# Performance work log

Measured on AMD Instinct MI355X. Metric: run time of the kernel, lower is better.

The kernel has to match this reference:

```python
import jax, jax.numpy as jnp
import numpy as np

B, S, D_MODEL, N_HEADS = 2, 256, 512, 8
HEAD_DIM = D_MODEL // N_HEADS  # 64; k.size(-1) used for scaling


def setup_inputs() -> dict:
    key = jax.random.key(0)
    ks = jax.random.split(key, 11)
    sd = 1.0 / np.sqrt(D_MODEL)
    sf = 1.0 / np.sqrt(N_HEADS * D_MODEL)
    return {
        "Q": jax.random.normal(ks[0], (B, S, D_MODEL), jnp.float32),
        "K": jax.random.normal(ks[1], (B, S, D_MODEL), jnp.float32),
        "V": jax.random.normal(ks[2], (B, S, D_MODEL), jnp.float32),
        "Wq": jax.random.normal(ks[3], (D_MODEL, D_MODEL * N_HEADS), jnp.float32) * sd,
        "bq": jax.random.normal(ks[4], (D_MODEL * N_HEADS,), jnp.float32) * sd,
        "Wk": jax.random.normal(ks[5], (D_MODEL, D_MODEL * N_HEADS), jnp.float32) * sd,
        "bk": jax.random.normal(ks[6], (D_MODEL * N_HEADS,), jnp.float32) * sd,
        "Wv": jax.random.normal(ks[7], (D_MODEL, D_MODEL * N_HEADS), jnp.float32) * sd,
        "bv": jax.random.normal(ks[8], (D_MODEL * N_HEADS,), jnp.float32) * sd,
        "Wf": jax.random.normal(ks[9], (N_HEADS * D_MODEL, D_MODEL), jnp.float32) * sf,
        "bf": jax.random.normal(ks[10], (D_MODEL,), jnp.float32) * sf,
    }


def _split_heads(x):
    # Faithful to torch: view(B, -1, n_heads, d_model//n_heads).transpose(1, 2).
    # x: (B, S, D_MODEL*N_HEADS) -> (B, N_HEADS, S*N_HEADS, HEAD_DIM)
    b = x.shape[0]
    return jnp.transpose(x.reshape(b, -1, N_HEADS, HEAD_DIM), (0, 2, 1, 3))


def reference(Q, K, V, Wq, bq, Wk, bk, Wv, bv, Wf, bf):
    q = _split_heads(Q @ Wq + bq)  # (B, H, S*H, Dh)
    k = _split_heads(K @ Wk + bk)
    v = _split_heads(V @ Wv + bv)
    scale = 1.0 / jnp.sqrt(jnp.float32(HEAD_DIM))
    scores = jnp.einsum("bhqd,bhkd->bhqk", q, k) * scale  # (B, H, S*H, S*H)
    weights = jax.nn.softmax(scores, axis=-1)
    ctx = jnp.einsum("bhqk,bhkd->bhqd", weights, v)  # (B, H, S*H, Dh)
    # transpose(1,2).view(B, -1, n_heads*d_model) -> (B, S, N_HEADS*D_MODEL)
    ctx = jnp.transpose(ctx, (0, 2, 1, 3)).reshape(Q.shape[0], -1, N_HEADS * D_MODEL)
    return ctx @ Wf + bf  # (B, S, D_MODEL)
```

## Files before the change

### kernel.cpp

```cpp
#include <hip/hip_runtime.h>
#include <hip/hip_bf16.h>


typedef __attribute__((ext_vector_type(4))) float f32x4;
typedef __attribute__((ext_vector_type(8))) short short8;
typedef __attribute__((ext_vector_type(4))) short short4v;
typedef __attribute__((ext_vector_type(4))) unsigned int u32x4;

#define SEQ 2048
#define DH 64
#define BH 16
#define ROWS 512
#define DM 512
#define NQ 4096
#define KSPLIT 8

static __device__ __forceinline__ unsigned short f2bf(float f) {
    return __builtin_bit_cast(unsigned short, __float2bfloat16(f));
}
static __device__ __forceinline__ short4v pk4(float a, float b, float c, float d) {
    return short4v{(short)f2bf(a), (short)f2bf(b), (short)f2bf(c), (short)f2bf(d)};
}
static __device__ __forceinline__ unsigned cvt_pk_bf16(float lo, float hi) {
    unsigned r;
    asm("v_cvt_pk_bf16_f32 %0, %1, %2" : "=v"(r) : "v"(lo), "v"(hi));
    return r;
}

__global__ __launch_bounds__(256) void qkv_proj_kernel(
    const float* __restrict__ Q, const float* __restrict__ K, const float* __restrict__ V,
    const float* __restrict__ Wq, const float* __restrict__ bq,
    const float* __restrict__ Wk, const float* __restrict__ bk,
    const float* __restrict__ Wv, const float* __restrict__ bv,
    unsigned short* __restrict__ q_bf, unsigned short* __restrict__ k_bf,
    unsigned short* __restrict__ vT_bf)
{
    const int mat = blockIdx.z;
    const float* X    = (mat == 0) ? Q  : (mat == 1) ? K  : V;
    const float* W    = (mat == 0) ? Wq : (mat == 1) ? Wk : Wv;
    const float* bias = (mat == 0) ? bq : (mat == 1) ? bk : bv;

    const int n0 = blockIdx.x * 64;
    const int m0 = blockIdx.y * 64;
    const int tid = threadIdx.x;
    const int w = tid >> 6, l = tid & 63;
    const int lr = l & 15, lg = l >> 4;

    __shared__ unsigned short a_lds[64][72];
    __shared__ unsigned short wt_lds[64 * 72];

    const int xr0 = tid >> 4, xc4 = (tid & 15) * 4;
    const int wn = tid & 63, wkseg = tid >> 6;
    const int wxr = (wn >> 3) & 7;

    f32x4 acc[4];
#pragma unroll
    for (int ct = 0; ct < 4; ++ct) acc[ct] = f32x4{0.f, 0.f, 0.f, 0.f};

    float4 rx[4];
    float rwv[16];

#pragma unroll
    for (int i = 0; i < 4; ++i)
        rx[i] = *reinterpret_cast<const float4*>(X + (m0 + i * 16 + xr0) * DM + xc4);
#pragma unroll
    for (int j = 0; j < 16; ++j)
        rwv[j] = W[(size_t)(wkseg * 16 + j) * NQ + n0 + wn];

    for (int t = 0; t < 8; ++t) {
#pragma unroll
        for (int i = 0; i < 4; ++i)
            *reinterpret_cast<short4v*>(&a_lds[i * 16 + xr0][xc4]) =
                pk4(rx[i].x, rx[i].y, rx[i].z, rx[i].w);
#pragma unroll
        for (int j4 = 0; j4 < 4; ++j4) {
            int kb = wkseg * 2 + (j4 >> 1);
            int off = wn * 72 + ((kb ^ wxr) << 3) + (j4 & 1) * 4;
            *reinterpret_cast<short4v*>(&wt_lds[off]) =
                pk4(rwv[j4 * 4 + 0], rwv[j4 * 4 + 1], rwv[j4 * 4 + 2], rwv[j4 * 4 + 3]);
        }
        __syncthreads();

        if (t < 7) {
            int k0 = (t + 1) * 64;
#pragma unroll
            for (int i = 0; i < 4; ++i)
                rx[i] = *reinterpret_cast<const float4*>(X + (m0 + i * 16 + xr0) * DM + k0 + xc4);
#pragma unroll
            for (int j = 0; j < 16; ++j)
                rwv[j] = W[(size_t)(k0 + wkseg * 16 + j) * NQ + n0 + wn];
        }

#pragma unroll
        for (int ks = 0; ks < 2; ++ks) {
            short8 a = *reinterpret_cast<const short8*>(&a_lds[w * 16 + lr][ks * 32 + lg * 8]);
#pragma unroll
            for (int ct = 0; ct < 4; ++ct) {
                int row = ct * 16 + lr;
                int kb = ks * 4 + lg;
                short8 b = *reinterpret_cast<const short8*>(
                    &wt_lds[row * 72 + ((kb ^ ((row >> 3) & 7)) << 3)]);
                acc[ct] = __builtin_amdgcn_mfma_f32_16x16x32_bf16(a, b, acc[ct], 0, 0, 0);
            }
        }
        __syncthreads();
    }

#pragma unroll
    for (int ct = 0; ct < 4; ++ct) {
        int c = n0 + ct * 16 + lr;
        float bv_ = bias[c];
        int h = (c >> 6) & 7, d = c & 63, c1 = c >> 9;
#pragma unroll
        for (int r = 0; r < 4; ++r) {
            int row = m0 + w * 16 + lg * 4 + r;
            int b = row >> 8, s = row & 255;
            int n = s * 8 + c1;
            unsigned short bfv = f2bf(acc[ct][r] + bv_);
            if (mat == 0)      q_bf[((b * 8 + h) * SEQ + n) * DH + d] = bfv;
            else if (mat == 1) k_bf[((b * 8 + h) * SEQ + n) * DH + d] = bfv;
            else               vT_bf[((b * 8 + h) * DH + d) * SEQ + n] = bfv;
        }
    }
}

__global__ __launch_bounds__(512, 4) void attn_kernel(
    const unsigned short* __restrict__ q_bf,
    const unsigned short* __restrict__ k_bf,
    const unsigned short* __restrict__ vT_bf,
    unsigned short* __restrict__ ctx_bf)
{
    const int bh = blockIdx.y;
    const int b = bh >> 3, h = bh & 7;
    const int n0 = blockIdx.x * 64;
    const int tid = threadIdx.x;
    const int w = tid >> 6, l = tid & 63;
    const int wq = w & 3, half = w >> 2;
    const int lr = l & 15, lg = l >> 4;
    const int gtid = tid & 255;

    const unsigned short* qb = q_bf + (size_t)bh * SEQ * DH;
    const unsigned short* kb = k_bf + (size_t)bh * SEQ * DH;
    const unsigned short* vb = vT_bf + (size_t)bh * DH * SEQ;

    __shared__ __align__(16) unsigned short kvl[4][64][72];
    __shared__ float l_red[4][16];

    const int qrow = n0 + wq * 16 + lr;
    short8 aq[2];
    aq[0] = *reinterpret_cast<const short8*>(qb + qrow * DH + lg * 8);
    aq[1] = *reinterpret_cast<const short8*>(qb + qrow * DH + 32 + lg * 8);

    f32x4 o[4];
#pragma unroll
    for (int i = 0; i < 4; ++i) o[i] = f32x4{0.f, 0.f, 0.f, 0.f};
    float l_part = 0.f;

    const int srow = gtid >> 3, sc8 = (gtid & 7) * 8;
    const int kbase0 = half * (SEQ / 2);

    short8 rk[2], rv[2];
#pragma unroll
    for (int i = 0; i < 2; ++i) {
        int row = srow + i * 32;
        rk[i] = *reinterpret_cast<const short8*>(kb + (kbase0 + row) * DH + sc8);
        rv[i] = *reinterpret_cast<const short8*>(vb + row * SEQ + kbase0 + sc8);
    }

    const bool lowc  = (lg < 2);
    const bool sendR = (lg == 0) || (lg == 3);
    const bool oddlg = (lg & 1);

    for (int kt = 0; kt < SEQ / 2 / 64; ++kt) {
#pragma unroll
        for (int i = 0; i < 2; ++i) {
            *reinterpret_cast<short8*>(&kvl[half][srow + i * 32][sc8]) = rk[i];
            *reinterpret_cast<short8*>(&kvl[2 + half][srow + i * 32][sc8]) = rv[i];
        }
        __syncthreads();

        if (kt < SEQ / 2 / 64 - 1) {
            int kb0 = kbase0 + (kt + 1) * 64;
#pragma unroll
            for (int i = 0; i < 2; ++i) {
                int row = srow + i * 32;
                rk[i] = *reinterpret_cast<const short8*>(kb + (kb0 + row) * DH + sc8);
                rv[i] = *reinterpret_cast<const short8*>(vb + row * SEQ + kb0 + sc8);
            }
        }

        f32x4 s[4];
#pragma unroll
        for (int ct = 0; ct < 4; ++ct) s[ct] = f32x4{0.f, 0.f, 0.f, 0.f};
#pragma unroll
        for (int ks = 0; ks < 2; ++ks) {
#pragma unroll
            for (int ct = 0; ct < 4; ++ct) {
                short8 kfrag = *reinterpret_cast<const short8*>(&kvl[half][ct * 16 + lr][ks * 32 + lg * 8]);
                s[ct] = __builtin_amdgcn_mfma_f32_16x16x32_bf16(kfrag, aq[ks], s[ct], 0, 0, 0);
            }
        }

        float rs_t = 0.f;
#pragma unroll
        for (int ct = 0; ct < 4; ++ct)
#pragma unroll
            for (int r = 0; r < 4; ++r) {
                float pv = exp2f(s[ct][r] * 0.18033688011112042f);
                s[ct][r] = pv;
                rs_t += pv;
            }
        l_part += rs_t;

        unsigned Wp[8];
#pragma unroll
        for (int c = 0; c < 4; ++c) {
            Wp[c * 2 + 0] = cvt_pk_bf16(s[c][0], s[c][1]);
            Wp[c * 2 + 1] = cvt_pk_bf16(s[c][2], s[c][3]);
        }

        unsigned keepA[4], r1r[4];
#pragma unroll
        for (int a = 0; a < 2; ++a)
#pragma unroll
            for (int hh = 0; hh < 2; ++hh) {
                int i = a * 2 + hh;
                unsigned snd = lowc ? Wp[(2 * a + 1) * 2 + hh] : Wp[(2 * a) * 2 + hh];
                keepA[i]     = lowc ? Wp[(2 * a) * 2 + hh]     : Wp[(2 * a + 1) * 2 + hh];
                r1r[i] = (unsigned)__shfl_xor((int)snd, 32);
            }
        unsigned r2k[4], r2r[4];
#pragma unroll
        for (int i = 0; i < 4; ++i) {
            unsigned snd = sendR ? r1r[i] : keepA[i];
            r2k[i]       = sendR ? keepA[i] : r1r[i];
            r2r[i] = (unsigned)__shfl_xor((int)snd, 16);
        }

        u32x4 pbu[2];
#pragma unroll
        for (int ks = 0; ks < 2; ++ks) {
            unsigned g0a = oddlg ? r2r[2 * ks + 0] : r2k[2 * ks + 0];
            unsigned g0b = oddlg ? r2r[2 * ks + 1] : r2k[2 * ks + 1];
            unsigned g1a = oddlg ? r2k[2 * ks + 0] : r2r[2 * ks + 0];
            unsigned g1b = oddlg ? r2k[2 * ks + 1] : r2r[2 * ks + 1];
            pbu[ks] = u32x4{g0a, g0b, g1a, g1b};
        }

#pragma unroll
        for (int ks = 0; ks < 2; ++ks) {
            short8 pfrag = __builtin_bit_cast(short8, pbu[ks]);
#pragma unroll
            for (int dt = 0; dt < 4; ++dt) {
                short8 vfrag = *reinterpret_cast<const short8*>(&kvl[2 + half][dt * 16 + lr][ks * 32 + lg * 8]);
                o[dt] = __builtin_amdgcn_mfma_f32_16x16x32_bf16(vfrag, pfrag, o[dt], 0, 0, 0);
            }
        }
        __syncthreads();
    }

    float rs = l_part;
    rs += __shfl_xor(rs, 16);
    rs += __shfl_xor(rs, 32);

    float* o_red = (float*)&kvl[0][0][0];
    const int orow = (wq * 16 + lr) * 72;
    if (half == 1) {
#pragma unroll
        for (int dt = 0; dt < 4; ++dt)
            *reinterpret_cast<f32x4*>(&o_red[orow + dt * 16 + lg * 4]) = o[dt];
        if (lg == 0) l_red[wq][lr] = rs;
    }
    __syncthreads();
    if (half == 0) {
        float inv = 1.f / (rs + l_red[wq][lr]);
        int n = n0 + wq * 16 + lr;
        int sp = n >> 3;
        int cbase = (n & 7) * 512 + h * 64;
        unsigned short* dst = ctx_bf + (size_t)(b * 256 + sp) * NQ + cbase;
#pragma unroll
        for (int dt = 0; dt < 4; ++dt) {
            f32x4 oo = *reinterpret_cast<f32x4*>(&o_red[orow + dt * 16 + lg * 4]);
            oo = (o[dt] + oo) * inv;
            *reinterpret_cast<short4v*>(dst + dt * 16 + lg * 4) = pk4(oo[0], oo[1], oo[2], oo[3]);
        }
    }
}

__global__ __launch_bounds__(256) void out_proj_splitk_kernel(
    const unsigned short* __restrict__ ctx_bf,
    const float* __restrict__ Wf,
    float* __restrict__ part)
{
    const int n0 = blockIdx.x * 64;
    const int m0 = blockIdx.y * 64;
    const int ksplit = blockIdx.z;
    const int kbase = ksplit * (NQ / KSPLIT);
    const int tid = threadIdx.x;
    const int w = tid >> 6, l = tid & 63;
    const int lr = l & 15, lg = l >> 4;

    __shared__ unsigned short a_lds[64][72];
    __shared__ unsigned short wt_lds[64 * 72];

    const int arow0 = tid >> 3, ac8 = (tid & 7) * 8;
    const int wn = tid & 63, wkseg = tid >> 6;
    const int wxr = (wn >> 3) & 7;

    f32x4 acc[4];
#pragma unroll
    for (int ct = 0; ct < 4; ++ct) acc[ct] = f32x4{0.f, 0.f, 0.f, 0.f};

    short8 ra[2];
    float rwv[16];

    {
#pragma unroll
        for (int i = 0; i < 2; ++i)
            ra[i] = *reinterpret_cast<const short8*>(
                ctx_bf + (size_t)(m0 + arow0 + i * 32) * NQ + kbase + ac8);
#pragma unroll
        for (int j = 0; j < 16; ++j)
            rwv[j] = Wf[(size_t)(kbase + wkseg * 16 + j) * DM + n0 + wn];
    }

    for (int t = 0; t < 8; ++t) {
#pragma unroll
        for (int i = 0; i < 2; ++i)
            *reinterpret_cast<short8*>(&a_lds[arow0 + i * 32][ac8]) = ra[i];
#pragma unroll
        for (int j4 = 0; j4 < 4; ++j4) {
            int kb = wkseg * 2 + (j4 >> 1);
            int off = wn * 72 + ((kb ^ wxr) << 3) + (j4 & 1) * 4;
            *reinterpret_cast<short4v*>(&wt_lds[off]) =
                pk4(rwv[j4 * 4 + 0], rwv[j4 * 4 + 1], rwv[j4 * 4 + 2], rwv[j4 * 4 + 3]);
        }
        __syncthreads();

        if (t < 7) {
            int k0 = kbase + (t + 1) * 64;
#pragma unroll
            for (int i = 0; i < 2; ++i)
                ra[i] = *reinterpret_cast<const short8*>(
                    ctx_bf + (size_t)(m0 + arow0 + i * 32) * NQ + k0 + ac8);
#pragma unroll
            for (int j = 0; j < 16; ++j)
                rwv[j] = Wf[(size_t)(k0 + wkseg * 16 + j) * DM + n0 + wn];
        }

#pragma unroll
        for (int ks = 0; ks < 2; ++ks) {
            short8 a = *reinterpret_cast<const short8*>(&a_lds[w * 16 + lr][ks * 32 + lg * 8]);
#pragma unroll
            for (int ct = 0; ct < 4; ++ct) {
                int row = ct * 16 + lr;
                int kb = ks * 4 + lg;
                short8 b = *reinterpret_cast<const short8*>(
                    &wt_lds[row * 72 + ((kb ^ ((row >> 3) & 7)) << 3)]);
                acc[ct] = __builtin_amdgcn_mfma_f32_16x16x32_bf16(a, b, acc[ct], 0, 0, 0);
            }
        }
        __syncthreads();
    }

    float* pbase = part + (size_t)ksplit * ROWS * DM;
#pragma unroll
    for (int ct = 0; ct < 4; ++ct) {
        int c = n0 + ct * 16 + lr;
#pragma unroll
        for (int r = 0; r < 4; ++r) {
            int row = m0 + w * 16 + lg * 4 + r;
            pbase[(size_t)row * DM + c] = acc[ct][r];
        }
    }
}

__global__ __launch_bounds__(256) void out_reduce_kernel(
    const float* __restrict__ part, const float* __restrict__ bf_,
    float* __restrict__ out)
{
    int i4 = blockIdx.x * 256 + threadIdx.x;
    int e = i4 * 4;
    float4 acc = *reinterpret_cast<const float4*>(bf_ + (e & (DM - 1)));
#pragma unroll
    for (int ks = 0; ks < KSPLIT; ++ks) {
        float4 p = *reinterpret_cast<const float4*>(part + (size_t)ks * ROWS * DM + e);
        acc.x += p.x; acc.y += p.y; acc.z += p.z; acc.w += p.w;
    }
    *reinterpret_cast<float4*>(out + e) = acc;
}

extern "C" void kernel_launch(void* const* d_in, const int* in_sizes, int n_in,
                              void* d_out, int out_size, void* d_ws, size_t ws_size,
                              hipStream_t stream) {
    const float* Q  = (const float*)d_in[0];
    const float* K  = (const float*)d_in[1];
    const float* V  = (const float*)d_in[2];
    const float* Wq = (const float*)d_in[3];
    const float* bq = (const float*)d_in[4];
    const float* Wk = (const float*)d_in[5];
    const float* bk = (const float*)d_in[6];
    const float* Wv = (const float*)d_in[7];
    const float* bv = (const float*)d_in[8];
    const float* Wf = (const float*)d_in[9];
    const float* bf = (const float*)d_in[10];
    float* out = (float*)d_out;

    unsigned short* q_bf  = (unsigned short*)d_ws;
    unsigned short* k_bf  = q_bf + (size_t)BH * SEQ * DH;
    unsigned short* vT_bf = k_bf + (size_t)BH * SEQ * DH;
    unsigned short* ctx_bf = vT_bf + (size_t)BH * SEQ * DH;
    float* part = (float*)d_ws;

    qkv_proj_kernel<<<dim3(NQ / 64, ROWS / 64, 3), 256, 0, stream>>>(
        Q, K, V, Wq, bq, Wk, bk, Wv, bv, q_bf, k_bf, vT_bf);
    attn_kernel<<<dim3(SEQ / 64, BH), 512, 0, stream>>>(q_bf, k_bf, vT_bf, ctx_bf);
    out_proj_splitk_kernel<<<dim3(DM / 64, ROWS / 64, KSPLIT), 256, 0, stream>>>(
        ctx_bf, Wf, part);
    out_reduce_kernel<<<dim3(ROWS * DM / 4 / 256), 256, 0, stream>>>(part, bf, out);
}
```

Measured before the change: 87.07 us.

## Split attention KV range across four wave groups per block instead of two

The attention block grows from 512 to 1024 threads. The key/value sequence is split into four quarters, each processed by its own group of four waves with its own shared-memory K/V tiles. Partial outputs and row sums from the three extra quarters are reduced through shared memory by the first group. This halves each block's sequential KV loop and adds in-block parallelism, at the cost of more LDS per block (lower block occupancy) and a larger final reduction.

Measured after the change: 157.9 us. 81.4% more time.

```diff
diff --git a/kernel.cpp b/kernel.cpp
--- a/kernel.cpp
+++ b/kernel.cpp
@@ -124,7 +124,7 @@
     }
 }
 
-__global__ __launch_bounds__(512, 4) void attn_kernel(
+__global__ __launch_bounds__(1024, 8) void attn_kernel(
     const unsigned short* __restrict__ q_bf,
     const unsigned short* __restrict__ k_bf,
     const unsigned short* __restrict__ vT_bf,
@@ -135,7 +135,7 @@
     const int n0 = blockIdx.x * 64;
     const int tid = threadIdx.x;
     const int w = tid >> 6, l = tid & 63;
-    const int wq = w & 3, half = w >> 2;
+    const int wq = w & 3, qtr = w >> 2;
     const int lr = l & 15, lg = l >> 4;
     const int gtid = tid & 255;
 
@@ -143,8 +143,8 @@
     const unsigned short* kb = k_bf + (size_t)bh * SEQ * DH;
     const unsigned short* vb = vT_bf + (size_t)bh * DH * SEQ;
 
-    __shared__ __align__(16) unsigned short kvl[4][64][72];
-    __shared__ float l_red[4][16];
+    __shared__ __align__(16) unsigned short kvl[8][64][72];
+    __shared__ float l_red[3][4][16];
 
     const int qrow = n0 + wq * 16 + lr;
     short8 aq[2];
@@ -157,7 +157,7 @@
     float l_part = 0.f;
 
     const int srow = gtid >> 3, sc8 = (gtid & 7) * 8;
-    const int kbase0 = half * (SEQ / 2);
+    const int kbase0 = qtr * (SEQ / 4);
 
     short8 rk[2], rv[2];
 #pragma unroll
@@ -171,15 +171,15 @@
     const bool sendR = (lg == 0) || (lg == 3);
     const bool oddlg = (lg & 1);
 
-    for (int kt = 0; kt < SEQ / 2 / 64; ++kt) {
+    for (int kt = 0; kt < SEQ / 4 / 64; ++kt) {
 #pragma unroll
         for (int i = 0; i < 2; ++i) {
-            *reinterpret_cast<short8*>(&kvl[half][srow + i * 32][sc8]) = rk[i];
-            *reinterpret_cast<short8*>(&kvl[2 + half][srow + i * 32][sc8]) = rv[i];
-        }
-        __syncthreads();
-
-        if (kt < SEQ / 2 / 64 - 1) {
+            *reinterpret_cast<short8*>(&kvl[qtr][srow + i * 32][sc8]) = rk[i];
+            *reinterpret_cast<short8*>(&kvl[4 + qtr][srow + i * 32][sc8]) = rv[i];
+        }
+        __syncthreads();
+
+        if (kt < SEQ / 4 / 64 - 1) {
             int kb0 = kbase0 + (kt + 1) * 64;
 #pragma unroll
             for (int i = 0; i < 2; ++i) {
@@ -196,7 +196,7 @@
         for (int ks = 0; ks < 2; ++ks) {
 #pragma unroll
             for (int ct = 0; ct < 4; ++ct) {
-                short8 kfrag = *reinterpret_cast<const short8*>(&kvl[half][ct * 16 + lr][ks * 32 + lg * 8]);
+                short8 kfrag = *reinterpret_cast<const short8*>(&kvl[qtr][ct * 16 + lr][ks * 32 + lg * 8]);
                 s[ct] = __builtin_amdgcn_mfma_f32_16x16x32_bf16(kfrag, aq[ks], s[ct], 0, 0, 0);
             }
         }
@@ -252,7 +252,7 @@
             short8 pfrag = __builtin_bit_cast(short8, pbu[ks]);
 #pragma unroll
             for (int dt = 0; dt < 4; ++dt) {
-                short8 vfrag = *reinterpret_cast<const short8*>(&kvl[2 + half][dt * 16 + lr][ks * 32 + lg * 8]);
+                short8 vfrag = *reinterpret_cast<const short8*>(&kvl[4 + qtr][dt * 16 + lr][ks * 32 + lg * 8]);
                 o[dt] = __builtin_amdgcn_mfma_f32_16x16x32_bf16(vfrag, pfrag, o[dt], 0, 0, 0);
             }
         }
@@ -264,24 +264,29 @@
     rs += __shfl_xor(rs, 32);
 
     float* o_red = (float*)&kvl[0][0][0];
-    const int orow = (wq * 16 + lr) * 72;
-    if (half == 1) {
+    if (qtr != 0) {
+        const int base = ((qtr - 1) * 4 + wq) * (16 * 72) + lr * 72;
 #pragma unroll
         for (int dt = 0; dt < 4; ++dt)
-            *reinterpret_cast<f32x4*>(&o_red[orow + dt * 16 + lg * 4]) = o[dt];
-        if (lg == 0) l_red[wq][lr] = rs;
+            *reinterpret_cast<f32x4*>(&o_red[base + dt * 16 + lg * 4]) = o[dt];
+        if (lg == 0) l_red[qtr - 1][wq][lr] = rs;
     }
     __syncthreads();
-    if (half == 0) {
-        float inv = 1.f / (rs + l_red[wq][lr]);
+    if (qtr == 0) {
+        float l_tot = rs + l_red[0][wq][lr] + l_red[1][wq][lr] + l_red[2][wq][lr];
+        float inv = 1.f / l_tot;
         int n = n0 + wq * 16 + lr;
         int sp = n >> 3;
         int cbase = (n & 7) * 512 + h * 64;
         unsigned short* dst = ctx_bf + (size_t)(b * 256 + sp) * NQ + cbase;
+        const int rbase = wq * (16 * 72) + lr * 72;
 #pragma unroll
         for (int dt = 0; dt < 4; ++dt) {
-            f32x4 oo = *reinterpret_cast<f32x4*>(&o_red[orow + dt * 16 + lg * 4]);
-            oo = (o[dt] + oo) * inv;
+            f32x4 oo = o[dt];
+#pragma unroll
+            for (int p = 0; p < 3; ++p)
+                oo += *reinterpret_cast<f32x4*>(&o_red[p * 4 * (16 * 72) + rbase + dt * 16 + lg * 4]);
+            oo *= inv;
             *reinterpret_cast<short4v*>(dst + dt * 16 + lg * 4) = pk4(oo[0], oo[1], oo[2], oo[3]);
         }
     }
@@ -414,7 +419,7 @@
 
     qkv_proj_kernel<<<dim3(NQ / 64, ROWS / 64, 3), 256, 0, stream>>>(
         Q, K, V, Wq, bq, Wk, bk, Wv, bv, q_bf, k_bf, vT_bf);
-    attn_kernel<<<dim3(SEQ / 64, BH), 512, 0, stream>>>(q_bf, k_bf, vT_bf, ctx_bf);
+    attn_kernel<<<dim3(SEQ / 64, BH), 1024, 0, stream>>>(q_bf, k_bf, vT_bf, ctx_bf);
     out_proj_splitk_kernel<<<dim3(DM / 64, ROWS / 64, KSPLIT), 256, 0, stream>>>(
         ctx_bf, Wf, part);
     out_reduce_kernel<<<dim3(ROWS * DM / 4 / 256), 256, 0, stream>>>(part, bf, out);
```

## Split attention over key range across two blocks and merge partials

Applied to the files above, without the earlier changes.

Adds an attention kernel that splits each query tile's key range into two halves handled by separate blocks (grid z=2). Each block writes unnormalized fp32 partial outputs and row sums to workspace, and a new merge kernel combines them and writes the bf16 context. The aim is to double the number of attention blocks and so improve occupancy and parallelism on the GPU. The cost is extra global traffic for the fp32 partials and one more kernel launch. The path depends on the workspace being large enough, and the original kernel stays as a fallback.

Result: slower. 93.14 us (+7.0%).

```diff
diff --git a/kernel.cpp b/kernel.cpp
--- a/kernel.cpp
+++ b/kernel.cpp
@@ -122,6 +122,191 @@
             else               vT_bf[((b * 8 + h) * DH + d) * SEQ + n] = bfv;
         }
     }
+}
+
+__global__ __launch_bounds__(512, 4) void attn_split_kernel(
+    const unsigned short* __restrict__ q_bf,
+    const unsigned short* __restrict__ k_bf,
+    const unsigned short* __restrict__ vT_bf,
+    float* __restrict__ po,
+    float* __restrict__ pl)
+{
+    const int bh = blockIdx.y;
+    const int z = blockIdx.z;
+    const int n0 = blockIdx.x * 64;
+    const int tid = threadIdx.x;
+    const int w = tid >> 6, l = tid & 63;
+    const int wq = w & 3, sub = w >> 2;
+    const int lr = l & 15, lg = l >> 4;
+    const int gtid = tid & 255;
+
+    po += (size_t)z * BH * SEQ * 64;
+    pl += (size_t)z * BH * SEQ;
+
+    const unsigned short* qb = q_bf + (size_t)bh * SEQ * DH;
+    const unsigned short* kb = k_bf + (size_t)bh * SEQ * DH;
+    const unsigned short* vb = vT_bf + (size_t)bh * DH * SEQ;
+
+    __shared__ __align__(16) unsigned short kvl[4][64][72];
+    __shared__ float l_red[4][16];
+
+    const int qrow = n0 + wq * 16 + lr;
+    short8 aq[2];
+    aq[0] = *reinterpret_cast<const short8*>(qb + qrow * DH + lg * 8);
+    aq[1] = *reinterpret_cast<const short8*>(qb + qrow * DH + 32 + lg * 8);
+
+    f32x4 o[4];
+#pragma unroll
+    for (int i = 0; i < 4; ++i) o[i] = f32x4{0.f, 0.f, 0.f, 0.f};
+    float l_part = 0.f;
+
+    const int srow = gtid >> 3, sc8 = (gtid & 7) * 8;
+    const int kbase0 = z * (SEQ / 2) + sub * (SEQ / 4);
+
+    short8 rk[2], rv[2];
+#pragma unroll
+    for (int i = 0; i < 2; ++i) {
+        int row = srow + i * 32;
+        rk[i] = *reinterpret_cast<const short8*>(kb + (kbase0 + row) * DH + sc8);
+        rv[i] = *reinterpret_cast<const short8*>(vb + row * SEQ + kbase0 + sc8);
+    }
+
+    const bool lowc  = (lg < 2);
+    const bool sendR = (lg == 0) || (lg == 3);
+    const bool oddlg = (lg & 1);
+
+    for (int kt = 0; kt < SEQ / 4 / 64; ++kt) {
+#pragma unroll
+        for (int i = 0; i < 2; ++i) {
+            *reinterpret_cast<short8*>(&kvl[sub][srow + i * 32][sc8]) = rk[i];
+            *reinterpret_cast<short8*>(&kvl[2 + sub][srow + i * 32][sc8]) = rv[i];
+        }
+        __syncthreads();
+
+        if (kt < SEQ / 4 / 64 - 1) {
+            int kb0 = kbase0 + (kt + 1) * 64;
+#pragma unroll
+            for (int i = 0; i < 2; ++i) {
+                int row = srow + i * 32;
+                rk[i] = *reinterpret_cast<const short8*>(kb + (kb0 + row) * DH + sc8);
+                rv[i] = *reinterpret_cast<const short8*>(vb + row * SEQ + kb0 + sc8);
+            }
+        }
+
+        f32x4 s[4];
+#pragma unroll
+        for (int ct = 0; ct < 4; ++ct) s[ct] = f32x4{0.f, 0.f, 0.f, 0.f};
+#pragma unroll
+        for (int ks = 0; ks < 2; ++ks) {
+#pragma unroll
+            for (int ct = 0; ct < 4; ++ct) {
+                short8 kfrag = *reinterpret_cast<const short8*>(&kvl[sub][ct * 16 + lr][ks * 32 + lg * 8]);
+                s[ct] = __builtin_amdgcn_mfma_f32_16x16x32_bf16(kfrag, aq[ks], s[ct], 0, 0, 0);
+            }
+        }
+
+        float rs_t = 0.f;
+#pragma unroll
+        for (int ct = 0; ct < 4; ++ct)
+#pragma unroll
+            for (int r = 0; r < 4; ++r) {
+                float pv = exp2f(s[ct][r] * 0.18033688011112042f);
+                s[ct][r] = pv;
+                rs_t += pv;
+            }
+        l_part += rs_t;
+
+        unsigned Wp[8];
+#pragma unroll
+        for (int c = 0; c < 4; ++c) {
+            Wp[c * 2 + 0] = cvt_pk_bf16(s[c][0], s[c][1]);
+            Wp[c * 2 + 1] = cvt_pk_bf16(s[c][2], s[c][3]);
+        }
+
+        unsigned keepA[4], r1r[4];
+#pragma unroll
+        for (int a = 0; a < 2; ++a)
+#pragma unroll
+            for (int hh = 0; hh < 2; ++hh) {
+                int i = a * 2 + hh;
+                unsigned snd = lowc ? Wp[(2 * a + 1) * 2 + hh] : Wp[(2 * a) * 2 + hh];
+                keepA[i]     = lowc ? Wp[(2 * a) * 2 + hh]     : Wp[(2 * a + 1) * 2 + hh];
+                r1r[i] = (unsigned)__shfl_xor((int)snd, 32);
+            }
+        unsigned r2k[4], r2r[4];
+#pragma unroll
+        for (int i = 0; i < 4; ++i) {
+            unsigned snd = sendR ? r1r[i] : keepA[i];
+            r2k[i]       = sendR ? keepA[i] : r1r[i];
+            r2r[i] = (unsigned)__shfl_xor((int)snd, 16);
+        }
+
+        u32x4 pbu[2];
+#pragma unroll
+        for (int ks = 0; ks < 2; ++ks) {
+            unsigned g0a = oddlg ? r2r[2 * ks + 0] : r2k[2 * ks + 0];
+            unsigned g0b = oddlg ? r2r[2 * ks + 1] : r2k[2 * ks + 1];
+            unsigned g1a = oddlg ? r2k[2 * ks + 0] : r2r[2 * ks + 0];
+            unsigned g1b = oddlg ? r2k[2 * ks + 1] : r2r[2 * ks + 1];
+            pbu[ks] = u32x4{g0a, g0b, g1a, g1b};
+        }
+
+#pragma unroll
+        for (int ks = 0; ks < 2; ++ks) {
+            short8 pfrag = __builtin_bit_cast(short8, pbu[ks]);
+#pragma unroll
+            for (int dt = 0; dt < 4; ++dt) {
+                short8 vfrag = *reinterpret_cast<const short8*>(&kvl[2 + sub][dt * 16 + lr][ks * 32 + lg * 8]);
+                o[dt] = __builtin_amdgcn_mfma_f32_16x16x32_bf16(vfrag, pfrag, o[dt], 0, 0, 0);
+            }
+        }
+        __syncthreads();
+    }
+
+    float rs = l_part;
+    rs += __shfl_xor(rs, 16);
+    rs += __shfl_xor(rs, 32);
+
+    float* o_red = (float*)&kvl[0][0][0];
+    const int orow = (wq * 16 + lr) * 72;
+    if (sub == 1) {
+#pragma unroll
+        for (int dt = 0; dt < 4; ++dt)
+            *reinterpret_cast<f32x4*>(&o_red[orow + dt * 16 + lg * 4]) = o[dt];
+        if (lg == 0) l_red[wq][lr] = rs;
+    }
+    __syncthreads();
+    if (sub == 0) {
+        float l_blk = rs + l_red[wq][lr];
+        int n = n0 + wq * 16 + lr;
+        size_t rbase = ((size_t)bh * SEQ + n) * 64;
+#pragma unroll
+        for (int dt = 0; dt < 4; ++dt) {
+            f32x4 oo = *reinterpret_cast<f32x4*>(&o_red[orow + dt * 16 + lg * 4]);
+            oo += o[dt];
+            *reinterpret_cast<f32x4*>(po + rbase + dt * 16 + lg * 4) = oo;
+        }
+        if (lg == 0) pl[bh * SEQ + n] = l_blk;
+    }
+}
+
+__global__ __launch_bounds__(256) void attn_merge_kernel(
+    const float* __restrict__ po,
+    const float* __restrict__ pl,
+    unsigned short* __restrict__ ctx_bf)
+{
+    int t = blockIdx.x * 256 + threadIdx.x;
+    int cg = t & 15, r = t >> 4;
+    const size_t Z = (size_t)BH * SEQ * 64;
+    float inv = 1.f / (pl[r] + pl[BH * SEQ + r]);
+    f32x4 a = *reinterpret_cast<const f32x4*>(po + (size_t)r * 64 + cg * 4);
+    f32x4 b = *reinterpret_cast<const f32x4*>(po + Z + (size_t)r * 64 + cg * 4);
+    a = (a + b) * inv;
+    int bh = r >> 11, n = r & (SEQ - 1);
+    int bb = bh >> 3, h = bh & 7, sp = n >> 3;
+    int cbase = (n & 7) * 512 + h * 64;
+    *reinterpret_cast<short4v*>(ctx_bf + (size_t)(bb * 256 + sp) * NQ + cbase + cg * 4) =
+        pk4(a[0], a[1], a[2], a[3]);
 }
 
 __global__ __launch_bounds__(512, 4) void attn_kernel(
@@ -174,8 +359,8 @@
     for (int kt = 0; kt < SEQ / 2 / 64; ++kt) {
 #pragma unroll
         for (int i = 0; i < 2; ++i) {
-            *reinterpret_cast<short8*>(&kvl[half][srow + i * 32][sc8]) = rk[i];
-            *reinterpret_cast<short8*>(&kvl[2 + half][srow + i * 32][sc8]) = rv[i];
+            *reinterpret_cast<short8*>(&kvl[half & 1][srow + i * 32][sc8]) = rk[i];
+            *reinterpret_cast<short8*>(&kvl[2 + (half & 1)][srow + i * 32][sc8]) = rv[i];
         }
         __syncthreads();
 
@@ -412,9 +597,22 @@
     unsigned short* ctx_bf = vT_bf + (size_t)BH * SEQ * DH;
     float* part = (float*)d_ws;
 
+    const size_t base16 = (size_t)BH * SEQ * DH * 3 * 2 + (size_t)ROWS * NQ * 2;
+    float* po = (float*)((char*)d_ws + base16);
+    float* pl = po + (size_t)2 * BH * SEQ * 64;
+    const size_t required = base16 + (size_t)2 * BH * SEQ * 64 * 4 + (size_t)2 * BH * SEQ * 4;
+
     qkv_proj_kernel<<<dim3(NQ / 64, ROWS / 64, 3), 256, 0, stream>>>(
         Q, K, V, Wq, bq, Wk, bk, Wv, bv, q_bf, k_bf, vT_bf);
-    attn_kernel<<<dim3(SEQ / 64, BH), 512, 0, stream>>>(q_bf, k_bf, vT_bf, ctx_bf);
+
+    if (ws_size >= required) {
+        attn_split_kernel<<<dim3(SEQ / 64, BH, 2), 512, 0, stream>>>(
+            q_bf, k_bf, vT_bf, po, pl);
+        attn_merge_kernel<<<dim3(BH * SEQ * 16 / 256), 256, 0, stream>>>(po, pl, ctx_bf);
+    } else {
+        attn_kernel<<<dim3(SEQ / 64, BH), 512, 0, stream>>>(q_bf, k_bf, vT_bf, ctx_bf);
+    }
+
     out_proj_splitk_kernel<<<dim3(DM / 64, ROWS / 64, KSPLIT), 256, 0, stream>>>(
         ctx_bf, Wf, part);
     out_reduce_kernel<<<dim3(ROWS * DM / 4 / 256), 256, 0, stream>>>(part, bf, out);
```
